# Kernel optimization log

Hardware: AMD Instinct MI355X
Metric: run time of the kernel (lower is better)

Reference implementation:

```python
import jax, jax.numpy as jnp
import numpy as np

EPS = 1e-6          # RMSNorm eps
SINK_EPS = 1e-12    # Sinkhorn denominator eps
N_ITER = 5          # sinkhorn_iters


def setup_inputs() -> dict:
    key = jax.random.key(0)
    ks = jax.random.split(key, 12)
    B, T, H, D = 2, 2048, 4, 2048
    FD = H * D
    W_SCALE = 0.02  # keep gate logits in a non-saturated sigmoid range
    return {
        "x": jax.random.normal(ks[0], (B, T, H, D), jnp.float32),
        "norm_w": jnp.ones((FD,), jnp.float32),
        "w_pre": jax.random.normal(ks[1], (H, FD), jnp.float32) * W_SCALE,
        "w_res": jax.random.normal(ks[2], (H * H, FD), jnp.float32) * W_SCALE,
        "w_post": jax.random.normal(ks[3], (H, FD), jnp.float32) * W_SCALE,
        "alpha_pre": jax.random.uniform(ks[4], (1,), jnp.float32),
        "alpha_res": jax.random.uniform(ks[5], (1,), jnp.float32),
        "alpha_post": jax.random.uniform(ks[6], (1,), jnp.float32),
        "s_pre": jax.random.normal(ks[7], (H,), jnp.float32),
        "s_res": jax.random.normal(ks[8], (H, H), jnp.float32),
        "s_post": jax.random.normal(ks[9], (H,), jnp.float32),
        "w_inner": jax.random.normal(ks[10], (D, D), jnp.float32) * (1.0 / np.sqrt(D)),
    }


def sinkhorn_knopp(logits, n_iter):
    # Doubly-stochastic projection over last two dims.
    m = jnp.exp(logits - jnp.max(logits, axis=(-2, -1), keepdims=True))
    for _ in range(n_iter):
        m = m / (jnp.sum(m, axis=-1, keepdims=True) + SINK_EPS)
        m = m / (jnp.sum(m, axis=-2, keepdims=True) + SINK_EPS)
    return m


def reference(x, norm_w, w_pre, w_res, w_post, alpha_pre, alpha_res, alpha_post,
              s_pre, s_res, s_post, w_inner):
    b, t, h, d = x.shape
    flat = x.reshape(b, t, h * d)
    # RMSNorm over flat dim
    var = jnp.mean(flat * flat, axis=-1, keepdims=True)
    normed = norm_w * flat * jax.lax.rsqrt(var + EPS)
    # Gate projections (Linear, no bias => x @ W.T)
    a_raw = alpha_pre * (normed @ w_pre.T) + s_pre                     # (b,t,h)
    b_raw = (alpha_res * (normed @ w_res.T)).reshape(b, t, h, h) + s_res
    c_raw = alpha_post * (normed @ w_post.T) + s_post                  # (b,t,h)
    a_l = jax.nn.sigmoid(a_raw)
    c_l = 2.0 * jax.nn.sigmoid(c_raw)
    b_l = sinkhorn_knopp(b_raw, N_ITER)
    # split: inner input
    inner_in = jnp.einsum('bth,bthd->btd', a_l, x)
    # inner layer: bias-free linear
    inner_out = inner_in @ w_inner.T
    # combine
    carry = jnp.einsum('bthk,btkd->bthd', b_l, x)
    write = jnp.einsum('bth,btd->bthd', c_l, inner_out)
    return carry + write
```

## Files before the change

### kernel.cpp

```cpp
#include <hip/hip_runtime.h>
#include <hip/hip_bf16.h>

#define FD 8192
#define DD 2048
#define NH 4
#define NT 4096
#define NG 24
#define NGP 32
#define KSPLIT 32
#define KC (FD / KSPLIT)
#define CH 64

typedef __attribute__((ext_vector_type(4))) float f32x4;
typedef __attribute__((ext_vector_type(8))) short short8;

__device__ inline unsigned short f2bf(float f) {
  __hip_bfloat16 h = __float2bfloat16(f);
  unsigned short u; __builtin_memcpy(&u, &h, 2); return u;
}
__device__ inline float bf2f(unsigned short u) {
  __hip_bfloat16 h; __builtin_memcpy(&h, &u, 2); return __bfloat162float(h);
}

__global__ __launch_bounds__(256) void k_prep(
    const float* __restrict__ w_inner,
    const float* __restrict__ w_pre,
    const float* __restrict__ w_res,
    const float* __restrict__ w_post,
    const float* __restrict__ norm_w,
    unsigned short* __restrict__ w_inner_bf,
    unsigned short* __restrict__ wnb)
{
  const int tid = threadIdx.x;
  const int wid = blockIdx.x * 256 + tid;
  f32x4 w4[4];
#pragma unroll
  for (int it = 0; it < 4; ++it) w4[it] = *(const f32x4*)&w_inner[wid * 16 + it * 4];
  __builtin_amdgcn_sched_barrier(0);
#pragma unroll
  for (int p = 0; p < 2; ++p) {
    f32x4 a = w4[2 * p], b = w4[2 * p + 1];
    short8 o;
    o[0] = (short)f2bf(a.x); o[1] = (short)f2bf(a.y);
    o[2] = (short)f2bf(a.z); o[3] = (short)f2bf(a.w);
    o[4] = (short)f2bf(b.x); o[5] = (short)f2bf(b.y);
    o[6] = (short)f2bf(b.z); o[7] = (short)f2bf(b.w);
    *(short8*)&w_inner_bf[wid * 16 + p * 8] = o;
  }
  {
    int j = wid >> 13, k = wid & (FD - 1);
    float w = (j < 4) ? w_pre[j * FD + k]
            : (j < 20) ? w_res[(j - 4) * FD + k]
            : (j < 24) ? w_post[(j - 20) * FD + k]
            : 0.0f;
    wnb[wid] = f2bf(w * norm_w[k]);
  }
}

__global__ __launch_bounds__(256) void k_gates(
    const float* __restrict__ x, const unsigned short* __restrict__ wnb,
    float* __restrict__ partial ,
    unsigned short* __restrict__ xb )
{
  __shared__ unsigned short xs[128][72];
  const int tb = blockIdx.x;
  const int ks = blockIdx.y;
  const int tid = threadIdx.x;
  const int wave = tid >> 6, lane = tid & 63;
  const int lr = lane & 15, kg = lane >> 4;
  const int t0 = tb * 128;
  const int k0 = ks * KC;
  const int sr = tid >> 4;
  const int sc = (tid & 15) * 4;

  float ssq8[8];
#pragma unroll
  for (int i = 0; i < 8; ++i) ssq8[i] = 0.f;
  f32x4 acc[2][2] = {};

  for (int ch = 0; ch < KC; ch += CH) {
    f32x4 v[8];
#pragma unroll
    for (int it = 0; it < 8; ++it)
      v[it] = *(const f32x4*)&x[(size_t)(t0 + it * 16 + sr) * FD + k0 + ch + sc];
    __builtin_amdgcn_sched_barrier(0);
    __syncthreads();
#pragma unroll
    for (int it = 0; it < 8; ++it) {
      f32x4 a = v[it];
      ssq8[it] += a.x * a.x + a.y * a.y + a.z * a.z + a.w * a.w;
      ushort4 o;
      o.x = f2bf(a.x); o.y = f2bf(a.y); o.z = f2bf(a.z); o.w = f2bf(a.w);
      int r = it * 16 + sr;
      *(ushort4*)&xs[r][sc] = o;
      *(ushort4*)&xb[(size_t)(t0 + r) * FD + k0 + ch + sc] = o;
    }
    __syncthreads();
#pragma unroll
    for (int kk = 0; kk < CH; kk += 32) {
      short8 a2[2], b2[2];
#pragma unroll
      for (int m = 0; m < 2; ++m)
        a2[m] = *(const short8*)&xs[wave * 32 + m * 16 + lr][kk + kg * 8];
#pragma unroll
      for (int n = 0; n < 2; ++n)
        b2[n] = *(const short8*)&wnb[(size_t)(n * 16 + lr) * FD + k0 + ch + kk + kg * 8];
#pragma unroll
      for (int m = 0; m < 2; ++m)
#pragma unroll
        for (int n = 0; n < 2; ++n)
          acc[m][n] = __builtin_amdgcn_mfma_f32_16x16x32_bf16(a2[m], b2[n], acc[m][n], 0, 0, 0);
    }
  }

  float* base = &partial[(size_t)ks * NT * (NG + 1)];
#pragma unroll
  for (int m = 0; m < 2; ++m)
#pragma unroll
    for (int n = 0; n < 2; ++n) {
      int g = n * 16 + lr;
      if (g < NG) {
#pragma unroll
        for (int r = 0; r < 4; ++r) {
          int row = wave * 32 + m * 16 + kg * 4 + r;
          base[(size_t)(t0 + row) * (NG + 1) + g] = acc[m][n][r];
        }
      }
    }
#pragma unroll
  for (int it = 0; it < 8; ++it) {
    float v = ssq8[it];
    v += __shfl_xor(v, 1);
    v += __shfl_xor(v, 2);
    v += __shfl_xor(v, 4);
    v += __shfl_xor(v, 8);
    if ((tid & 15) == 0) {
      int row = it * 16 + sr;
      base[(size_t)(t0 + row) * (NG + 1) + NG] = v;
    }
  }
}

__global__ __launch_bounds__(256) void k_scalars(
    const float* __restrict__ partial,
    const float* __restrict__ alpha_pre, const float* __restrict__ alpha_res,
    const float* __restrict__ alpha_post,
    const float* __restrict__ s_pre, const float* __restrict__ s_res,
    const float* __restrict__ s_post,
    float* __restrict__ gates )
{
  int t = blockIdx.x * blockDim.x + threadIdx.x;
  if (t >= NT) return;
  float acc[NG + 1];
#pragma unroll
  for (int j = 0; j <= NG; ++j) acc[j] = 0.f;
  for (int s = 0; s < KSPLIT; ++s) {
    const float* p = &partial[((size_t)s * NT + t) * (NG + 1)];
#pragma unroll
    for (int j = 0; j <= NG; ++j) acc[j] += p[j];
  }
  float rinv = rsqrtf(acc[NG] * (1.0f / FD) + 1e-6f);
  float ap = alpha_pre[0], ar = alpha_res[0], apo = alpha_post[0];

  float out[NG];
#pragma unroll
  for (int h = 0; h < 4; ++h)
    out[h] = 1.f / (1.f + expf(-(ap * rinv * acc[h] + s_pre[h])));
#pragma unroll
  for (int h = 0; h < 4; ++h)
    out[4 + h] = 2.f / (1.f + expf(-(apo * rinv * acc[20 + h] + s_post[h])));

  float m[16]; float mx = -1e30f;
#pragma unroll
  for (int j = 0; j < 16; ++j) {
    float br = ar * rinv * acc[4 + j] + s_res[j];
    m[j] = br; mx = fmaxf(mx, br);
  }
#pragma unroll
  for (int j = 0; j < 16; ++j) m[j] = expf(m[j] - mx);
#pragma unroll
  for (int it = 0; it < 5; ++it) {
#pragma unroll
    for (int h = 0; h < 4; ++h) {
      float rs = m[h*4] + m[h*4+1] + m[h*4+2] + m[h*4+3];
      float inv = 1.f / (rs + 1e-12f);
      m[h*4] *= inv; m[h*4+1] *= inv; m[h*4+2] *= inv; m[h*4+3] *= inv;
    }
#pragma unroll
    for (int k = 0; k < 4; ++k) {
      float cs = m[k] + m[4+k] + m[8+k] + m[12+k];
      float inv = 1.f / (cs + 1e-12f);
      m[k] *= inv; m[4+k] *= inv; m[8+k] *= inv; m[12+k] *= inv;
    }
  }
#pragma unroll
  for (int j = 0; j < 16; ++j) out[8 + j] = m[j];

  float* gt = &gates[(size_t)t * 24];
#pragma unroll
  for (int j = 0; j < NG; ++j) gt[j] = out[j];
}

__global__ __launch_bounds__(256) void k_inner_in(
    const unsigned short* __restrict__ xb, const float* __restrict__ gates,
    unsigned short* __restrict__ inner_in)
{
  int t = blockIdx.x, tid = threadIdx.x;
  const float* g = &gates[(size_t)t * 24];
  float a0 = g[0], a1 = g[1], a2 = g[2], a3 = g[3];
  const unsigned short* xt = &xb[(size_t)t * FD];
  int d = tid * 8;
  short8 h0 = *(const short8*)&xt[0 * DD + d];
  short8 h1 = *(const short8*)&xt[1 * DD + d];
  short8 h2 = *(const short8*)&xt[2 * DD + d];
  short8 h3 = *(const short8*)&xt[3 * DD + d];
  short8 o;
#pragma unroll
  for (int j = 0; j < 8; ++j) {
    float s = a0 * bf2f((unsigned short)h0[j]) + a1 * bf2f((unsigned short)h1[j])
            + a2 * bf2f((unsigned short)h2[j]) + a3 * bf2f((unsigned short)h3[j]);
    o[j] = (short)f2bf(s);
  }
  *(short8*)&inner_in[(size_t)t * DD + d] = o;
}

__global__ __launch_bounds__(256) void k_gemm(
    const unsigned short* __restrict__ A,
    const unsigned short* __restrict__ B,
    unsigned short* __restrict__ C)
{
  __shared__ unsigned short As[128 * 64];
  __shared__ unsigned short Bs[128 * 64];
  const int bid = blockIdx.x;
  const int bm = bid >> 4, bn = bid & 15;
  const int tid = threadIdx.x;
  const int wave = tid >> 6, lane = tid & 63;
  const int wm = wave >> 1, wn_ = wave & 1;
  const int lr = lane & 15, kg = lane >> 4;

  const int srow = tid >> 3;
  const int scol = (tid & 7) * 8;
  const unsigned short* a_src = &A[(size_t)(bm * 128 + srow) * 2048 + scol];
  const unsigned short* b_src = &B[(size_t)(bn * 128 + srow) * 2048 + scol];

  f32x4 acc[4][4] = {};

  for (int kt = 0; kt < 2048; kt += 64) {
    __syncthreads();
#pragma unroll
    for (int it = 0; it < 4; ++it)
      __builtin_amdgcn_global_load_lds(
          (const __attribute__((address_space(1))) void*)(a_src + (size_t)it * 32 * 2048 + kt),
          (__attribute__((address_space(3))) void*)(&As[it * 2048 + tid * 8]), 16, 0, 0);
#pragma unroll
    for (int it = 0; it < 4; ++it)
      __builtin_amdgcn_global_load_lds(
          (const __attribute__((address_space(1))) void*)(b_src + (size_t)it * 32 * 2048 + kt),
          (__attribute__((address_space(3))) void*)(&Bs[it * 2048 + tid * 8]), 16, 0, 0);
    __syncthreads();
#pragma unroll
    for (int kk = 0; kk < 64; kk += 32) {
      short8 a[4], b[4];
#pragma unroll
      for (int m = 0; m < 4; ++m)
        a[m] = *(const short8*)&As[(wm * 64 + m * 16 + lr) * 64 + kk + kg * 8];
#pragma unroll
      for (int n = 0; n < 4; ++n)
        b[n] = *(const short8*)&Bs[(wn_ * 64 + n * 16 + lr) * 64 + kk + kg * 8];
#pragma unroll
      for (int m = 0; m < 4; ++m)
#pragma unroll
        for (int n = 0; n < 4; ++n)
          acc[m][n] = __builtin_amdgcn_mfma_f32_16x16x32_bf16(a[m], b[n], acc[m][n], 0, 0, 0);
    }
  }

  const int row_base = bm * 128 + wm * 64;
  const int col_base = bn * 128 + wn_ * 64;
#pragma unroll
  for (int m = 0; m < 4; ++m)
#pragma unroll
    for (int n = 0; n < 4; ++n) {
      int col = col_base + n * 16 + lr;
#pragma unroll
      for (int r = 0; r < 4; ++r) {
        int row = row_base + m * 16 + kg * 4 + r;
        C[(size_t)row * 2048 + col] = f2bf(acc[m][n][r]);
      }
    }
}

__global__ __launch_bounds__(256) void k_out(
    const unsigned short* __restrict__ xb, const float* __restrict__ gates,
    const unsigned short* __restrict__ inner_out, float* __restrict__ out)
{
  int t = blockIdx.x, tid = threadIdx.x;
  const float* g = &gates[(size_t)t * 24];
  float c[4], bl[16];
#pragma unroll
  for (int h = 0; h < 4; ++h) c[h] = g[4 + h];
#pragma unroll
  for (int j = 0; j < 16; ++j) bl[j] = g[8 + j];
  const unsigned short* xt = &xb[(size_t)t * FD];
  float* ot = &out[(size_t)t * FD];
  int d = tid * 8;
  short8 xh[4];
#pragma unroll
  for (int h = 0; h < 4; ++h) xh[h] = *(const short8*)&xt[h * DD + d];
  short8 iu = *(const short8*)&inner_out[(size_t)t * DD + d];
  float io[8], xf[4][8];
#pragma unroll
  for (int j = 0; j < 8; ++j) io[j] = bf2f((unsigned short)iu[j]);
#pragma unroll
  for (int h = 0; h < 4; ++h)
#pragma unroll
    for (int j = 0; j < 8; ++j) xf[h][j] = bf2f((unsigned short)xh[h][j]);
#pragma unroll
  for (int h = 0; h < 4; ++h) {
    f32x4 o0, o1;
#pragma unroll
    for (int j = 0; j < 4; ++j) {
      o0[j] = c[h] * io[j]     + bl[h*4+0] * xf[0][j]     + bl[h*4+1] * xf[1][j]
                               + bl[h*4+2] * xf[2][j]     + bl[h*4+3] * xf[3][j];
      o1[j] = c[h] * io[j + 4] + bl[h*4+0] * xf[0][j + 4] + bl[h*4+1] * xf[1][j + 4]
                               + bl[h*4+2] * xf[2][j + 4] + bl[h*4+3] * xf[3][j + 4];
    }
    *(f32x4*)&ot[h * DD + d] = o0;
    *(f32x4*)&ot[h * DD + d + 4] = o1;
  }
}

extern "C" void kernel_launch(void* const* d_in, const int* in_sizes, int n_in,
                              void* d_out, int out_size, void* d_ws, size_t ws_size,
                              hipStream_t stream) {
  const float* x          = (const float*)d_in[0];
  const float* norm_w     = (const float*)d_in[1];
  const float* w_pre      = (const float*)d_in[2];
  const float* w_res      = (const float*)d_in[3];
  const float* w_post     = (const float*)d_in[4];
  const float* alpha_pre  = (const float*)d_in[5];
  const float* alpha_res  = (const float*)d_in[6];
  const float* alpha_post = (const float*)d_in[7];
  const float* s_pre      = (const float*)d_in[8];
  const float* s_res      = (const float*)d_in[9];
  const float* s_post     = (const float*)d_in[10];
  const float* w_inner    = (const float*)d_in[11];
  float* out = (float*)d_out;

  char* ws = (char*)d_ws;
  size_t top = ws_size & ~(size_t)255;
  auto alloc_top = [&](size_t bytes) -> void* {
    top = (top - bytes) & ~(size_t)255;
    return ws + top;
  };
  unsigned short* xb         = (unsigned short*)alloc_top((size_t)NT * FD * 2);
  float* partial = (float*)alloc_top((size_t)KSPLIT * NT * (NG + 1) * 4);
  unsigned short* w_inner_bf = (unsigned short*)alloc_top((size_t)DD * DD * 2);
  unsigned short* inner_in   = (unsigned short*)alloc_top((size_t)NT * DD * 2);
  unsigned short* inner_out  = (unsigned short*)alloc_top((size_t)NT * DD * 2);
  unsigned short* wnb        = (unsigned short*)alloc_top((size_t)NGP * FD * 2);
  float* gates   = (float*)alloc_top((size_t)NT * 24 * 4);

  k_prep<<<1024, 256, 0, stream>>>(w_inner, w_pre, w_res, w_post, norm_w, w_inner_bf, wnb);
  k_gates<<<dim3(32, 32), 256, 0, stream>>>(x, wnb, partial, xb);
  k_scalars<<<16, 256, 0, stream>>>(partial, alpha_pre, alpha_res, alpha_post,
                                    s_pre, s_res, s_post, gates);
  k_inner_in<<<4096, 256, 0, stream>>>(xb, gates, inner_in);
  k_gemm<<<512, 256, 0, stream>>>(inner_in, w_inner_bf, inner_out);
  k_out<<<4096, 256, 0, stream>>>(xb, gates, inner_out, out);
}
```

Baseline: 173.3 us.

## Fuse output combine into GEMM epilogue and drop inner_out buffer

Moves the final carry+write combine (Sinkhorn-mixed x plus gated inner output) into the GEMM epilogue, staging per-row gates in shared memory. This removes the bf16 inner_out intermediate write/read and the separate k_out launch. In exchange, the epilogue performs scalar 2-byte xb loads and 4-byte fp32 stores in the MFMA accumulator layout, which are less coalesced than the old vectorized k_out accesses.

```diff
diff --git a/kernel.cpp b/kernel.cpp
--- a/kernel.cpp
+++ b/kernel.cpp
@@ -227,10 +227,13 @@
 __global__ __launch_bounds__(256) void k_gemm(
     const unsigned short* __restrict__ A,
     const unsigned short* __restrict__ B,
-    unsigned short* __restrict__ C)
+    const unsigned short* __restrict__ xb,
+    const float* __restrict__ gates,
+    float* __restrict__ out)
 {
   __shared__ unsigned short As[128 * 64];
   __shared__ unsigned short Bs[128 * 64];
+  __shared__ float sg[128][20];
   const int bid = blockIdx.x;
   const int bm = bid >> 4, bn = bid & 15;
   const int tid = threadIdx.x;
@@ -238,6 +241,14 @@
   const int wm = wave >> 1, wn_ = wave & 1;
   const int lr = lane & 15, kg = lane >> 4;
 
+  {
+    int row = tid >> 1;
+    int half = (tid & 1) * 10;
+    const float* gp = &gates[(size_t)(bm * 128 + row) * 24 + 4];
+#pragma unroll
+    for (int j = 0; j < 10; ++j) sg[row][half + j] = gp[half + j];
+  }
+
   const int srow = tid >> 3;
   const int scol = (tid & 7) * 8;
   const unsigned short* a_src = &A[(size_t)(bm * 128 + srow) * 2048 + scol];
@@ -275,59 +286,31 @@
     }
   }
 
-  const int row_base = bm * 128 + wm * 64;
   const int col_base = bn * 128 + wn_ * 64;
 #pragma unroll
   for (int m = 0; m < 4; ++m)
 #pragma unroll
     for (int n = 0; n < 4; ++n) {
-      int col = col_base + n * 16 + lr;
+      int gcol = col_base + n * 16 + lr;
 #pragma unroll
       for (int r = 0; r < 4; ++r) {
-        int row = row_base + m * 16 + kg * 4 + r;
-        C[(size_t)row * 2048 + col] = f2bf(acc[m][n][r]);
+        int trow = wm * 64 + m * 16 + kg * 4 + r;
+        size_t tg = (size_t)(bm * 128 + trow);
+        float av = acc[m][n][r];
+        float xk[4];
+#pragma unroll
+        for (int k = 0; k < 4; ++k)
+          xk[k] = bf2f(xb[tg * FD + k * DD + gcol]);
+        const float* g = sg[trow];
+#pragma unroll
+        for (int h = 0; h < 4; ++h) {
+          float val = g[h] * av
+                    + g[4 + h * 4 + 0] * xk[0] + g[4 + h * 4 + 1] * xk[1]
+                    + g[4 + h * 4 + 2] * xk[2] + g[4 + h * 4 + 3] * xk[3];
+          out[tg * FD + h * DD + gcol] = val;
+        }
       }
     }
-}
-
-__global__ __launch_bounds__(256) void k_out(
-    const unsigned short* __restrict__ xb, const float* __restrict__ gates,
-    const unsigned short* __restrict__ inner_out, float* __restrict__ out)
-{
-  int t = blockIdx.x, tid = threadIdx.x;
-  const float* g = &gates[(size_t)t * 24];
-  float c[4], bl[16];
-#pragma unroll
-  for (int h = 0; h < 4; ++h) c[h] = g[4 + h];
-#pragma unroll
-  for (int j = 0; j < 16; ++j) bl[j] = g[8 + j];
-  const unsigned short* xt = &xb[(size_t)t * FD];
-  float* ot = &out[(size_t)t * FD];
-  int d = tid * 8;
-  short8 xh[4];
-#pragma unroll
-  for (int h = 0; h < 4; ++h) xh[h] = *(const short8*)&xt[h * DD + d];
-  short8 iu = *(const short8*)&inner_out[(size_t)t * DD + d];
-  float io[8], xf[4][8];
-#pragma unroll
-  for (int j = 0; j < 8; ++j) io[j] = bf2f((unsigned short)iu[j]);
-#pragma unroll
-  for (int h = 0; h < 4; ++h)
-#pragma unroll
-    for (int j = 0; j < 8; ++j) xf[h][j] = bf2f((unsigned short)xh[h][j]);
-#pragma unroll
-  for (int h = 0; h < 4; ++h) {
-    f32x4 o0, o1;
-#pragma unroll
-    for (int j = 0; j < 4; ++j) {
-      o0[j] = c[h] * io[j]     + bl[h*4+0] * xf[0][j]     + bl[h*4+1] * xf[1][j]
-                               + bl[h*4+2] * xf[2][j]     + bl[h*4+3] * xf[3][j];
-      o1[j] = c[h] * io[j + 4] + bl[h*4+0] * xf[0][j + 4] + bl[h*4+1] * xf[1][j + 4]
-                               + bl[h*4+2] * xf[2][j + 4] + bl[h*4+3] * xf[3][j + 4];
-    }
-    *(f32x4*)&ot[h * DD + d] = o0;
-    *(f32x4*)&ot[h * DD + d + 4] = o1;
-  }
 }
 
 extern "C" void kernel_launch(void* const* d_in, const int* in_sizes, int n_in,
@@ -357,7 +340,6 @@
   float* partial = (float*)alloc_top((size_t)KSPLIT * NT * (NG + 1) * 4);
   unsigned short* w_inner_bf = (unsigned short*)alloc_top((size_t)DD * DD * 2);
   unsigned short* inner_in   = (unsigned short*)alloc_top((size_t)NT * DD * 2);
-  unsigned short* inner_out  = (unsigned short*)alloc_top((size_t)NT * DD * 2);
   unsigned short* wnb        = (unsigned short*)alloc_top((size_t)NGP * FD * 2);
   float* gates   = (float*)alloc_top((size_t)NT * 24 * 4);
 
@@ -366,6 +348,5 @@
   k_scalars<<<16, 256, 0, stream>>>(partial, alpha_pre, alpha_res, alpha_post,
                                     s_pre, s_res, s_post, gates);
   k_inner_in<<<4096, 256, 0, stream>>>(xb, gates, inner_in);
-  k_gemm<<<512, 256, 0, stream>>>(inner_in, w_inner_bf, inner_out);
-  k_out<<<4096, 256, 0, stream>>>(xb, gates, inner_out, out);
-}
+  k_gemm<<<512, 256, 0, stream>>>(inner_in, w_inner_bf, xb, gates, out);
+}
```

After: 201.2 us. 1.16x slower.
